# Kernel optimization log

Measured on AMD Instinct MI355X. Metric: run time of the kernel, lower is better.

Reference implementation:

```python
import jax, jax.numpy as jnp
import numpy as np

N_NODES = 4096   # nodes in propagation tree
WORDS = 64       # word indices per node (bag-of-words)
HID = 256        # hidden_dim
VOCAB = 50257    # word_dim
NCLASS = 4
N_LEAF = 2048


def setup_inputs() -> dict:
    key = jax.random.key(0)
    ks = jax.random.split(key, 16)
    s = jnp.float32(0.1)  # init_matrix scale
    tree = jax.random.randint(ks[0], (N_NODES, WORDS), 0, VOCAB, dtype=jnp.int32)
    # parent[i] < i so node_h[parent] is already computed (topological order)
    parent = jax.random.randint(ks[1], (N_NODES,), 0, N_NODES, dtype=jnp.int32)
    parent = jnp.minimum(parent, jnp.maximum(jnp.arange(N_NODES, dtype=jnp.int32) - 1, 0))
    edge = jnp.stack([parent, jnp.arange(N_NODES, dtype=jnp.int32)], axis=1)
    leaf_idxs = jax.random.randint(ks[2], (N_LEAF,), 0, N_NODES, dtype=jnp.int32)
    y = jax.random.uniform(ks[3], (NCLASS,), dtype=jnp.float32)
    E = jax.random.normal(ks[4], (HID, VOCAB), dtype=jnp.float32) * s
    W_z = jax.random.normal(ks[5], (HID, HID), dtype=jnp.float32) * s
    U_z = jax.random.normal(ks[6], (HID, HID), dtype=jnp.float32) * s
    W_r = jax.random.normal(ks[7], (HID, HID), dtype=jnp.float32) * s
    U_r = jax.random.normal(ks[8], (HID, HID), dtype=jnp.float32) * s
    W_h = jax.random.normal(ks[9], (HID, HID), dtype=jnp.float32) * s
    U_h = jax.random.normal(ks[10], (HID, HID), dtype=jnp.float32) * s
    W_out = jax.random.normal(ks[11], (NCLASS, HID), dtype=jnp.float32) * s
    b_z = jnp.zeros((HID,), jnp.float32)
    b_r = jnp.zeros((HID,), jnp.float32)
    b_h = jnp.zeros((HID,), jnp.float32)
    b_out = jnp.zeros((NCLASS,), jnp.float32)
    return dict(tree=tree, edge=edge, leaf_idxs=leaf_idxs, y=y, E=E,
                W_z=W_z, U_z=U_z, b_z=b_z, W_r=W_r, U_r=U_r, b_r=b_r,
                W_h=W_h, U_h=U_h, b_h=b_h, W_out=W_out, b_out=b_out)


def reference(tree, edge, leaf_idxs, y, E, W_z, U_z, b_z, W_r, U_r, b_r,
              W_h, U_h, b_h, W_out, b_out):
    n_nodes = tree.shape[0]
    # child_xe per node: sum of word embeddings -> [N, HID]
    X = jnp.take(E, tree, axis=1).sum(axis=-1).T
    # W.mul(x).sum(dim=1) == W @ x; precompute input-side matvecs for all nodes
    WzX = X @ W_z.T
    WrX = X @ W_r.T
    WhX = X @ W_h.T
    node_h0 = jnp.zeros((n_nodes, X.shape[1]), X.dtype).at[0].set(X[0])

    def step(node_h, inp):
        i, wzx, wrx, whx, p = inp
        ph = node_h[p]  # parent hidden state
        z = jax.nn.sigmoid(wzx + U_z @ ph + b_z)
        r = jax.nn.sigmoid(wrx + U_r @ ph + b_r)
        c = jnp.tanh(whx + U_h @ (ph * r) + b_h)
        h = z * ph + (1.0 - z) * c
        return node_h.at[i].set(h), None

    xs = (jnp.arange(1, n_nodes), WzX[1:], WrX[1:], WhX[1:], edge[1:, 0])
    node_h, _ = jax.lax.scan(step, node_h0, xs)
    final_state = node_h[leaf_idxs].max(axis=0)  # [HID]
    pred = jax.nn.softmax(W_out @ final_state + b_out)
    loss = jnp.sum((y - pred) ** 2)
    return pred, loss
```

## Files before the change

### kernel.cpp

```cpp
#include <hip/hip_runtime.h>
#include <math.h>

#define N_NODES 4096
#define WORDS   64
#define HID     256
#define VOCAB   50257
#define NCLASS  4
#define N_LEAF  2048
#define RNN_BLOCKS 256
#define POISON 0x7FFF7FFFu

typedef _Float16 half2_t __attribute__((ext_vector_type(2)));

__device__ __forceinline__ float dot2f(half2_t a, half2_t b, float c) {
#if __has_builtin(__builtin_amdgcn_fdot2)
  return __builtin_amdgcn_fdot2(a, b, c, false);
#else
  return c + (float)a.x * (float)b.x + (float)a.y * (float)b.y;
#endif
}

__device__ __forceinline__ half2_t f2h2(float f) {
  union { float f; half2_t h; } u; u.f = f; return u.h;
}

__device__ __forceinline__ float fast_rcp(float x) { return __builtin_amdgcn_rcpf(x); }
__device__ __forceinline__ float fast_sigmoid(float x) {
  return fast_rcp(1.f + __expf(-x));
}
__device__ __forceinline__ float fast_tanh(float x) {
  return 1.f - 2.f * fast_rcp(1.f + __expf(2.f * x));
}
__device__ __forceinline__ half2_t pkrtz(float a, float b) {
#if __has_builtin(__builtin_amdgcn_cvt_pkrtz)
  return __builtin_bit_cast(half2_t, __builtin_amdgcn_cvt_pkrtz(a, b));
#else
  half2_t v; v.x = (_Float16)a; v.y = (_Float16)b; return v;
#endif
}

__global__ void poison_hpk_kernel(unsigned* __restrict__ HpkU) {
  int i = blockIdx.x * blockDim.x + threadIdx.x;
  if (i < N_NODES * (HID / 2)) HpkU[i] = POISON;
}

__global__ void transpose_f16_kernel(const float* __restrict__ src, _Float16* __restrict__ dst,
                                     int R, int C) {
  __shared__ float tile[32][33];
  int c0 = blockIdx.x * 32, r0 = blockIdx.y * 32;
  int tx = threadIdx.x, ty = threadIdx.y;
#pragma unroll
  for (int j = 0; j < 32; j += 8) {
    int c = c0 + tx, r = r0 + ty + j;
    if (c < C) tile[ty + j][tx] = src[(size_t)r * C + c];
  }
  __syncthreads();
#pragma unroll
  for (int j = 0; j < 32; j += 8) {
    int c = c0 + ty + j, r = r0 + tx;
    if (c < C) dst[(size_t)c * R + r] = (_Float16)tile[tx][ty + j];
  }
}

__global__ void __launch_bounds__(256) pack_u_kernel(
    const float* __restrict__ Uz, const float* __restrict__ Ur, const float* __restrict__ Uh,
    half2_t* __restrict__ Upk) {
  __shared__ float tile[64][259];
  int m = blockIdx.x >> 2, g = blockIdx.x & 3;
  const float* U = m == 0 ? Uz : (m == 1 ? Ur : Uh);
  int t = threadIdx.x;
  for (int r = 0; r < 64; ++r) tile[r][t] = U[(size_t)(g * 64 + r) * 256 + t];
  __syncthreads();
#pragma unroll
  for (int it = 0; it < 32; ++it) {
    int e = it * 256 + t;
    int hl = e & 63, kj = e >> 6, s = kj >> 5, j = kj & 31;
    half2_t v;
    v.x = (_Float16)tile[hl][s * 64 + 2 * j];
    v.y = (_Float16)tile[hl][s * 64 + 2 * j + 1];
    Upk[(size_t)(m * 4 + s) * 8192 + j * 256 + (g * 64 + hl)] = v;
  }
}

__global__ void gather_x_kernel(const int* __restrict__ tree, const half2_t* __restrict__ ETh2,
                                float* __restrict__ X, float* __restrict__ H,
                                half2_t* __restrict__ Hpk) {
  int i = blockIdx.x;
  int t = threadIdx.x;
  __shared__ int vs[WORDS];
  if (t < WORDS) vs[t] = tree[i * WORDS + t];
  __syncthreads();
  float ax = 0.f, ay = 0.f;
#pragma unroll 8
  for (int w = 0; w < WORDS; ++w) {
    half2_t e = ETh2[(size_t)vs[w] * (HID / 2) + t];
    ax += (float)e.x;
    ay += (float)e.y;
  }
  float2 v2; v2.x = ax; v2.y = ay;
  ((float2*)(X + (size_t)i * HID))[t] = v2;
  if (i == 0) {
    ((float2*)H)[t] = v2;
    half2_t hv; hv.x = (_Float16)ax; hv.y = (_Float16)ay;
    Hpk[t] = hv;
  }
}

__global__ void __launch_bounds__(256) gemm3_kernel(
    const float* __restrict__ X,
    const float* __restrict__ W0, const float* __restrict__ W1, const float* __restrict__ W2,
    float* __restrict__ A0, float* __restrict__ A1, float* __restrict__ A2) {
  const float* W = blockIdx.z == 0 ? W0 : (blockIdx.z == 1 ? W1 : W2);
  float*       A = blockIdx.z == 0 ? A0 : (blockIdx.z == 1 ? A1 : A2);
  __shared__ float Xs[16][65];
  __shared__ float Ws[16][65];
  int tid = threadIdx.x;
  int m0 = blockIdx.x * 64, n0 = blockIdx.y * 64;
  int tm = (tid / 16) * 4, tn = (tid % 16) * 4;
  int lm = tid >> 2, lk = (tid & 3) * 4;
  float acc[4][4];
#pragma unroll
  for (int a = 0; a < 4; ++a)
#pragma unroll
    for (int b = 0; b < 4; ++b) acc[a][b] = 0.f;

  for (int k0 = 0; k0 < HID; k0 += 16) {
    float4 xv = *(const float4*)(X + (size_t)(m0 + lm) * HID + k0 + lk);
    Xs[lk + 0][lm] = xv.x; Xs[lk + 1][lm] = xv.y; Xs[lk + 2][lm] = xv.z; Xs[lk + 3][lm] = xv.w;
    float4 wv = *(const float4*)(W + (size_t)(n0 + lm) * HID + k0 + lk);
    Ws[lk + 0][lm] = wv.x; Ws[lk + 1][lm] = wv.y; Ws[lk + 2][lm] = wv.z; Ws[lk + 3][lm] = wv.w;
    __syncthreads();
#pragma unroll
    for (int k = 0; k < 16; ++k) {
      float xm[4], wn[4];
#pragma unroll
      for (int u = 0; u < 4; ++u) { xm[u] = Xs[k][tm + u]; wn[u] = Ws[k][tn + u]; }
#pragma unroll
      for (int a = 0; a < 4; ++a)
#pragma unroll
        for (int b = 0; b < 4; ++b) acc[a][b] = fmaf(xm[a], wn[b], acc[a][b]);
    }
    __syncthreads();
  }
#pragma unroll
  for (int a = 0; a < 4; ++a)
#pragma unroll
    for (int b = 0; b < 4; ++b)
      A[(size_t)(m0 + tm + a) * HID + n0 + tn + b] = acc[a][b];
}

__global__ void
__attribute__((amdgpu_flat_work_group_size(512, 512), amdgpu_waves_per_eu(2, 2)))
rnn_kernel(
    const float* __restrict__ Az, const float* __restrict__ Ar, const float* __restrict__ Ah,
    const half2_t* __restrict__ Upk,
    const float* __restrict__ bz, const float* __restrict__ br, const float* __restrict__ bh,
    const int* __restrict__ edge, float* __restrict__ H, unsigned* HpkU) {
  const int tid = threadIdx.x;
  const int h   = tid & (HID - 1);
  const int ks  = tid >> 8;
  __shared__ half2_t php[HID / 2];
  __shared__ half2_t rhp[HID / 2];
  __shared__ float   part[2 * HID];

  half2_t um[128];
  half2_t uhh[64];
  {
    const half2_t* mb = Upk + (size_t)(ks ? 4 : 0) * 8192 + h;
#pragma unroll
    for (int j = 0; j < 128; ++j)
      um[j] = mb[(j >> 5) * 8192 + (j & 31) * 256];
    const half2_t* hb = Upk + (size_t)(8 + 2 * ks) * 8192 + h;
#pragma unroll
    for (int j = 0; j < 64; ++j)
      uhh[j] = hb[(j >> 5) * 8192 + (j & 31) * 256];
  }
  const float b1  = ks ? br[h] : bz[h];
  const float bhv = ks ? 0.f : bh[h];

  const int istart = blockIdx.x == 0 ? RNN_BLOCKS : blockIdx.x;
  for (int i = istart; i < N_NODES; i += RNN_BLOCKS) {
    const int p = edge[2 * i];
    const float a1 = ks ? Ar[(size_t)i * HID + h] : Az[(size_t)i * HID + h];
    const float a2 = ks ? 0.f : Ah[(size_t)i * HID + h];

    if (tid < HID / 2) {
      unsigned v = __hip_atomic_load(&HpkU[(size_t)p * (HID / 2) + tid],
                                     __ATOMIC_RELAXED, __HIP_MEMORY_SCOPE_AGENT);
      long spin = 0;
      while (v == POISON) {
        if (++spin > (1L << 26)) break;
        v = __hip_atomic_load(&HpkU[(size_t)p * (HID / 2) + tid],
                              __ATOMIC_RELAXED, __HIP_MEMORY_SCOPE_AGENT);
      }
      php[tid] = __builtin_bit_cast(half2_t, v);
    }
    __syncthreads();

    half2_t ph2 = php[h >> 1];
    const float phv = (float)((h & 1) ? ph2.y : ph2.x);

    float ac0 = a1 + b1, ac1 = 0.f, ac2 = 0.f, ac3 = 0.f;
    {
      const float4* phq = (const float4*)php;
#pragma unroll
      for (int q = 0; q < 32; ++q) {
        float4 blk = phq[q];
        ac0 = dot2f(um[4 * q + 0], f2h2(blk.x), ac0);
        ac1 = dot2f(um[4 * q + 1], f2h2(blk.y), ac1);
        ac2 = dot2f(um[4 * q + 2], f2h2(blk.z), ac2);
        ac3 = dot2f(um[4 * q + 3], f2h2(blk.w), ac3);
      }
    }
    const float g = fast_sigmoid((ac0 + ac1) + (ac2 + ac3));
    if (ks) {
      float rh = g * phv;
      float nb = __shfl_xor(rh, 1, 64);
      if ((h & 1) == 0) rhp[h >> 1] = pkrtz(rh, nb);
    }
    __syncthreads();

    float c0 = 0.f, c1 = 0.f;
    {
      const float4* rq = (const float4*)(rhp + ks * 64);
#pragma unroll
      for (int q = 0; q < 16; ++q) {
        float4 blk = rq[q];
        c0 = dot2f(uhh[4 * q + 0], f2h2(blk.x), c0);
        c1 = dot2f(uhh[4 * q + 1], f2h2(blk.y), c1);
        c0 = dot2f(uhh[4 * q + 2], f2h2(blk.z), c0);
        c1 = dot2f(uhh[4 * q + 3], f2h2(blk.w), c1);
      }
    }
    part[ks * HID + h] = c0 + c1;
    __syncthreads();

    if (ks == 0) {
      float ca = a2 + bhv + part[h] + part[HID + h];
      float c  = fast_tanh(ca);
      float hn = fmaf(g, phv, (1.f - g) * c);
      float nb = __shfl_xor(hn, 1, 64);
      if ((h & 1) == 0) {
        __hip_atomic_store(&HpkU[(size_t)i * (HID / 2) + (h >> 1)],
                           __builtin_bit_cast(unsigned, pkrtz(hn, nb)),
                           __ATOMIC_RELAXED, __HIP_MEMORY_SCOPE_AGENT);
      }
      H[(size_t)i * HID + h] = hn;
    }
  }
}

__global__ void leafmax_kernel(const float* __restrict__ H, const int* __restrict__ leafs,
                               float* __restrict__ partial) {
  int b = blockIdx.x;
  int h = threadIdx.x;
  float m = -INFINITY;
#pragma unroll 4
  for (int j = 0; j < N_LEAF / 64; ++j) {
    int node = leafs[b * (N_LEAF / 64) + j];
    m = fmaxf(m, H[(size_t)node * HID + h]);
  }
  partial[b * HID + h] = m;
}

__global__ void final_kernel(const float* __restrict__ partial, const float* __restrict__ W_out,
                             const float* __restrict__ b_out, const float* __restrict__ y,
                             float* __restrict__ out) {
  int h = threadIdx.x;
  float m = -INFINITY;
#pragma unroll 8
  for (int b = 0; b < 64; ++b) m = fmaxf(m, partial[b * HID + h]);
  __shared__ float fs[HID];
  __shared__ float red[HID];
  __shared__ float logit[NCLASS];
  fs[h] = m;
  __syncthreads();
  for (int c = 0; c < NCLASS; ++c) {
    red[h] = W_out[c * HID + h] * fs[h];
    __syncthreads();
    for (int s = HID / 2; s > 0; s >>= 1) {
      if (h < s) red[h] += red[h + s];
      __syncthreads();
    }
    if (h == 0) logit[c] = red[0] + b_out[c];
    __syncthreads();
  }
  if (h == 0) {
    float mx = logit[0];
    for (int c = 1; c < NCLASS; ++c) mx = fmaxf(mx, logit[c]);
    float e[NCLASS], s = 0.f;
    for (int c = 0; c < NCLASS; ++c) { e[c] = expf(logit[c] - mx); s += e[c]; }
    float loss = 0.f;
    for (int c = 0; c < NCLASS; ++c) {
      float p = e[c] / s;
      out[c] = p;
      float d = y[c] - p;
      loss += d * d;
    }
    out[NCLASS] = loss;
  }
}

extern "C" void kernel_launch(void* const* d_in, const int* in_sizes, int n_in,
                              void* d_out, int out_size, void* d_ws, size_t ws_size,
                              hipStream_t stream) {
  const int*   tree = (const int*)d_in[0];
  const int*   edge = (const int*)d_in[1];
  const int*   leaf = (const int*)d_in[2];
  const float* y    = (const float*)d_in[3];
  const float* E    = (const float*)d_in[4];
  const float* Wz   = (const float*)d_in[5];
  const float* Uz   = (const float*)d_in[6];
  const float* bz   = (const float*)d_in[7];
  const float* Wr   = (const float*)d_in[8];
  const float* Ur   = (const float*)d_in[9];
  const float* br   = (const float*)d_in[10];
  const float* Wh   = (const float*)d_in[11];
  const float* Uh   = (const float*)d_in[12];
  const float* bh   = (const float*)d_in[13];
  const float* Wout = (const float*)d_in[14];
  const float* bout = (const float*)d_in[15];
  float* out = (float*)d_out;

  char* base = (char*)d_ws;
  size_t b = 0;
  _Float16* ETh = (_Float16*)(base + b); b += (size_t)VOCAB * HID * 2;
  b = (b + 255) & ~(size_t)255;
  half2_t* Upk = (half2_t*)(base + b); b += (size_t)3 * 4 * 8192 * 4;
  half2_t* Hpk = (half2_t*)(base + b); b += (size_t)N_NODES * (HID / 2) * 4;
  float* X   = (float*)(base + b); b += (size_t)N_NODES * HID * 4;
  float* Az  = (float*)(base + b); b += (size_t)N_NODES * HID * 4;
  float* Ar  = (float*)(base + b); b += (size_t)N_NODES * HID * 4;
  float* Ah  = (float*)(base + b); b += (size_t)N_NODES * HID * 4;
  float* H   = (float*)(base + b); b += (size_t)N_NODES * HID * 4;
  float* partial = (float*)(base + b); b += (size_t)64 * HID * 4;

  poison_hpk_kernel<<<(N_NODES * (HID / 2) + 255) / 256, 256, 0, stream>>>((unsigned*)Hpk);
  transpose_f16_kernel<<<dim3((VOCAB + 31) / 32, HID / 32), dim3(32, 8), 0, stream>>>(E, ETh, HID, VOCAB);
  pack_u_kernel<<<12, 256, 0, stream>>>(Uz, Ur, Uh, Upk);
  gather_x_kernel<<<N_NODES, 128, 0, stream>>>(tree, (const half2_t*)ETh, X, H, Hpk);
  gemm3_kernel<<<dim3(N_NODES / 64, HID / 64, 3), 256, 0, stream>>>(X, Wz, Wr, Wh, Az, Ar, Ah);
  rnn_kernel<<<RNN_BLOCKS, 512, 0, stream>>>(Az, Ar, Ah, Upk, bz, br, bh, edge, H, (unsigned*)Hpk);
  leafmax_kernel<<<64, HID, 0, stream>>>(H, leaf, partial);
  final_kernel<<<1, HID, 0, stream>>>(partial, Wout, bout, y, out);
}
```

Baseline: 538.4 us.

## Chain-follow consecutive child nodes in-block to bypass global spin handoff

After a block computes node j, it checks whether node j+1 has j as parent and has not yet been published. If so, it computes j+1 itself, reusing the just-computed hidden state from LDS instead of waiting for another block to poll it from global memory. Blocks also skip nodes that another block has already published. The intent is to shorten the sequential critical path on long parent chains by removing cross-block latency. The cost is extra atomic checks, redundant computation when two blocks race on the same node, and a sync hazard on the php rewrite.

```diff
diff --git a/kernel.cpp b/kernel.cpp
--- a/kernel.cpp
+++ b/kernel.cpp
@@ -162,6 +162,8 @@
   __shared__ half2_t php[HID / 2];
   __shared__ half2_t rhp[HID / 2];
   __shared__ float   part[2 * HID];
+  __shared__ int     sskip;
+  __shared__ int     sfol;
 
   half2_t um[128];
   half2_t uhh[64];
@@ -180,72 +182,100 @@
 
   const int istart = blockIdx.x == 0 ? RNN_BLOCKS : blockIdx.x;
   for (int i = istart; i < N_NODES; i += RNN_BLOCKS) {
-    const int p = edge[2 * i];
-    const float a1 = ks ? Ar[(size_t)i * HID + h] : Az[(size_t)i * HID + h];
-    const float a2 = ks ? 0.f : Ah[(size_t)i * HID + h];
-
-    if (tid < HID / 2) {
-      unsigned v = __hip_atomic_load(&HpkU[(size_t)p * (HID / 2) + tid],
-                                     __ATOMIC_RELAXED, __HIP_MEMORY_SCOPE_AGENT);
-      long spin = 0;
-      while (v == POISON) {
-        if (++spin > (1L << 26)) break;
-        v = __hip_atomic_load(&HpkU[(size_t)p * (HID / 2) + tid],
-                              __ATOMIC_RELAXED, __HIP_MEMORY_SCOPE_AGENT);
-      }
-      php[tid] = __builtin_bit_cast(half2_t, v);
-    }
-    __syncthreads();
-
-    half2_t ph2 = php[h >> 1];
-    const float phv = (float)((h & 1) ? ph2.y : ph2.x);
-
-    float ac0 = a1 + b1, ac1 = 0.f, ac2 = 0.f, ac3 = 0.f;
-    {
-      const float4* phq = (const float4*)php;
-#pragma unroll
-      for (int q = 0; q < 32; ++q) {
-        float4 blk = phq[q];
-        ac0 = dot2f(um[4 * q + 0], f2h2(blk.x), ac0);
-        ac1 = dot2f(um[4 * q + 1], f2h2(blk.y), ac1);
-        ac2 = dot2f(um[4 * q + 2], f2h2(blk.z), ac2);
-        ac3 = dot2f(um[4 * q + 3], f2h2(blk.w), ac3);
-      }
-    }
-    const float g = fast_sigmoid((ac0 + ac1) + (ac2 + ac3));
-    if (ks) {
-      float rh = g * phv;
-      float nb = __shfl_xor(rh, 1, 64);
-      if ((h & 1) == 0) rhp[h >> 1] = pkrtz(rh, nb);
-    }
-    __syncthreads();
-
-    float c0 = 0.f, c1 = 0.f;
-    {
-      const float4* rq = (const float4*)(rhp + ks * 64);
-#pragma unroll
-      for (int q = 0; q < 16; ++q) {
-        float4 blk = rq[q];
-        c0 = dot2f(uhh[4 * q + 0], f2h2(blk.x), c0);
-        c1 = dot2f(uhh[4 * q + 1], f2h2(blk.y), c1);
-        c0 = dot2f(uhh[4 * q + 2], f2h2(blk.z), c0);
-        c1 = dot2f(uhh[4 * q + 3], f2h2(blk.w), c1);
-      }
-    }
-    part[ks * HID + h] = c0 + c1;
-    __syncthreads();
-
-    if (ks == 0) {
-      float ca = a2 + bhv + part[h] + part[HID + h];
-      float c  = fast_tanh(ca);
-      float hn = fmaf(g, phv, (1.f - g) * c);
-      float nb = __shfl_xor(hn, 1, 64);
-      if ((h & 1) == 0) {
-        __hip_atomic_store(&HpkU[(size_t)i * (HID / 2) + (h >> 1)],
-                           __builtin_bit_cast(unsigned, pkrtz(hn, nb)),
-                           __ATOMIC_RELAXED, __HIP_MEMORY_SCOPE_AGENT);
-      }
-      H[(size_t)i * HID + h] = hn;
+    int j = i;
+    int p = edge[2 * j];
+    float a1 = ks ? Ar[(size_t)j * HID + h] : Az[(size_t)j * HID + h];
+    float a2 = ks ? 0.f : Ah[(size_t)j * HID + h];
+    bool useLds = false;
+
+    while (true) {
+      if (!useLds) {
+        if (tid == 0)
+          sskip = (__hip_atomic_load(&HpkU[(size_t)j * (HID / 2)],
+                                     __ATOMIC_RELAXED, __HIP_MEMORY_SCOPE_AGENT) != POISON);
+        if (tid < HID / 2) {
+          unsigned v = __hip_atomic_load(&HpkU[(size_t)p * (HID / 2) + tid],
+                                         __ATOMIC_RELAXED, __HIP_MEMORY_SCOPE_AGENT);
+          long spin = 0;
+          while (v == POISON) {
+            if (++spin > (1L << 26)) break;
+            v = __hip_atomic_load(&HpkU[(size_t)p * (HID / 2) + tid],
+                                  __ATOMIC_RELAXED, __HIP_MEMORY_SCOPE_AGENT);
+          }
+          php[tid] = __builtin_bit_cast(half2_t, v);
+        }
+      } else if (tid == 0) {
+        sskip = 0;
+      }
+      __syncthreads();
+      if (sskip) break;
+
+      const int jn = j + 1;
+      int pn = -1; unsigned pubw = 0u; float a1n = 0.f, a2n = 0.f;
+      if (jn < N_NODES) {
+        pn  = edge[2 * jn];
+        a1n = ks ? Ar[(size_t)jn * HID + h] : Az[(size_t)jn * HID + h];
+        a2n = ks ? 0.f : Ah[(size_t)jn * HID + h];
+        if (tid == 0)
+          pubw = __hip_atomic_load(&HpkU[(size_t)jn * (HID / 2)],
+                                   __ATOMIC_RELAXED, __HIP_MEMORY_SCOPE_AGENT);
+      }
+      if (tid == 0) sfol = (jn < N_NODES) && (pn == j) && (pubw == POISON);
+
+      half2_t ph2 = php[h >> 1];
+      const float phv = (float)((h & 1) ? ph2.y : ph2.x);
+
+      float ac0 = a1 + b1, ac1 = 0.f, ac2 = 0.f, ac3 = 0.f;
+      {
+        const float4* phq = (const float4*)php;
+#pragma unroll
+        for (int q = 0; q < 32; ++q) {
+          float4 blk = phq[q];
+          ac0 = dot2f(um[4 * q + 0], f2h2(blk.x), ac0);
+          ac1 = dot2f(um[4 * q + 1], f2h2(blk.y), ac1);
+          ac2 = dot2f(um[4 * q + 2], f2h2(blk.z), ac2);
+          ac3 = dot2f(um[4 * q + 3], f2h2(blk.w), ac3);
+        }
+      }
+      const float g = fast_sigmoid((ac0 + ac1) + (ac2 + ac3));
+      if (ks) {
+        float rh = g * phv;
+        float nb = __shfl_xor(rh, 1, 64);
+        if ((h & 1) == 0) rhp[h >> 1] = pkrtz(rh, nb);
+      }
+      __syncthreads();
+
+      float c0 = 0.f, c1 = 0.f;
+      {
+        const float4* rq = (const float4*)(rhp + ks * 64);
+#pragma unroll
+        for (int q = 0; q < 16; ++q) {
+          float4 blk = rq[q];
+          c0 = dot2f(uhh[4 * q + 0], f2h2(blk.x), c0);
+          c1 = dot2f(uhh[4 * q + 1], f2h2(blk.y), c1);
+          c0 = dot2f(uhh[4 * q + 2], f2h2(blk.z), c0);
+          c1 = dot2f(uhh[4 * q + 3], f2h2(blk.w), c1);
+        }
+      }
+      part[ks * HID + h] = c0 + c1;
+      __syncthreads();
+
+      const int fol = sfol;
+      if (ks == 0) {
+        float ca = a2 + bhv + part[h] + part[HID + h];
+        float c  = fast_tanh(ca);
+        float hn = fmaf(g, phv, (1.f - g) * c);
+        float nb = __shfl_xor(hn, 1, 64);
+        if ((h & 1) == 0) {
+          unsigned pk = __builtin_bit_cast(unsigned, pkrtz(hn, nb));
+          __hip_atomic_store(&HpkU[(size_t)j * (HID / 2) + (h >> 1)], pk,
+                             __ATOMIC_RELAXED, __HIP_MEMORY_SCOPE_AGENT);
+          if (fol) php[h >> 1] = __builtin_bit_cast(half2_t, pk);
+        }
+        H[(size_t)j * HID + h] = hn;
+      }
+      if (!fol) break;
+      j = jn; a1 = a1n; a2 = a2n; useLds = true;
     }
   }
 }
```

Measured after the change: 643.1 us. 1.19x slower.

## Repartition RNN gate work across half-blocks and prefetch next parent state

Applied to the files above, without the earlier changes.

The GRU step's matrix work is re-split between the two 256-thread halves. One half computes U_r and half of U_z, while the other computes the full U_h plus the other half of U_z. This removes the partial-sum reduction barrier, going from three syncthreads per step to two. The half that does not produce h now prefetches the next node's parent state, spinning on the poison flag, along with the next Ar, and the other half prefetches the next Az/Ah. This overlaps global latency with compute but risks load imbalance between the halves, and it lowers the spin timeout.

```diff
diff --git a/kernel.cpp b/kernel.cpp
--- a/kernel.cpp
+++ b/kernel.cpp
@@ -161,84 +161,106 @@
   const int ks  = tid >> 8;
   __shared__ half2_t php[HID / 2];
   __shared__ half2_t rhp[HID / 2];
-  __shared__ float   part[2 * HID];
-
-  half2_t um[128];
-  half2_t uhh[64];
+  __shared__ float   zh[HID];
+
+  half2_t big[128];
+  half2_t small[64];
   {
-    const half2_t* mb = Upk + (size_t)(ks ? 4 : 0) * 8192 + h;
+    const half2_t* mb = Upk + (size_t)(ks ? 4 : 8) * 8192 + h;
 #pragma unroll
     for (int j = 0; j < 128; ++j)
-      um[j] = mb[(j >> 5) * 8192 + (j & 31) * 256];
-    const half2_t* hb = Upk + (size_t)(8 + 2 * ks) * 8192 + h;
+      big[j] = mb[(j >> 5) * 8192 + (j & 31) * 256];
+    const half2_t* sb = Upk + (size_t)(ks ? 2 : 0) * 8192 + h;
 #pragma unroll
     for (int j = 0; j < 64; ++j)
-      uhh[j] = hb[(j >> 5) * 8192 + (j & 31) * 256];
-  }
-  const float b1  = ks ? br[h] : bz[h];
+      small[j] = sb[(j >> 5) * 8192 + (j & 31) * 256];
+  }
+  const float bzv = ks ? 0.f : bz[h];
   const float bhv = ks ? 0.f : bh[h];
-
-  const int istart = blockIdx.x == 0 ? RNN_BLOCKS : blockIdx.x;
-  for (int i = istart; i < N_NODES; i += RNN_BLOCKS) {
-    const int p = edge[2 * i];
-    const float a1 = ks ? Ar[(size_t)i * HID + h] : Az[(size_t)i * HID + h];
-    const float a2 = ks ? 0.f : Ah[(size_t)i * HID + h];
-
-    if (tid < HID / 2) {
-      unsigned v = __hip_atomic_load(&HpkU[(size_t)p * (HID / 2) + tid],
+  const float brv = ks ? br[h] : 0.f;
+
+  const int i0 = (blockIdx.x == 0) ? RNN_BLOCKS : blockIdx.x;
+  const int tl = tid - HID;
+
+  float az = 0.f, ah = 0.f, ar = 0.f;
+  if (!ks) {
+    az = Az[(size_t)i0 * HID + h];
+    ah = Ah[(size_t)i0 * HID + h];
+  } else {
+    ar = Ar[(size_t)i0 * HID + h];
+    const int p = edge[2 * i0];
+    if (tl < HID / 2) {
+      unsigned v = __hip_atomic_load(&HpkU[(size_t)p * (HID / 2) + tl],
                                      __ATOMIC_RELAXED, __HIP_MEMORY_SCOPE_AGENT);
       long spin = 0;
       while (v == POISON) {
-        if (++spin > (1L << 26)) break;
-        v = __hip_atomic_load(&HpkU[(size_t)p * (HID / 2) + tid],
+        if (++spin > (1L << 22)) break;
+        v = __hip_atomic_load(&HpkU[(size_t)p * (HID / 2) + tl],
                               __ATOMIC_RELAXED, __HIP_MEMORY_SCOPE_AGENT);
       }
-      php[tid] = __builtin_bit_cast(half2_t, v);
-    }
-    __syncthreads();
-
+      php[tl] = __builtin_bit_cast(half2_t, v);
+    }
+  }
+
+  for (int i = i0; i < N_NODES; i += RNN_BLOCKS) {
+    __syncthreads();
     half2_t ph2 = php[h >> 1];
     const float phv = (float)((h & 1) ? ph2.y : ph2.x);
-
-    float ac0 = a1 + b1, ac1 = 0.f, ac2 = 0.f, ac3 = 0.f;
-    {
-      const float4* phq = (const float4*)php;
+    const float4* phq = (const float4*)php;
+
+    float z0 = 0.f, z1 = 0.f, z2 = 0.f, z3 = 0.f;
+    float r0 = 0.f, r1 = 0.f, r2 = 0.f, r3 = 0.f;
+    if (ks) {
 #pragma unroll
       for (int q = 0; q < 32; ++q) {
         float4 blk = phq[q];
-        ac0 = dot2f(um[4 * q + 0], f2h2(blk.x), ac0);
-        ac1 = dot2f(um[4 * q + 1], f2h2(blk.y), ac1);
-        ac2 = dot2f(um[4 * q + 2], f2h2(blk.z), ac2);
-        ac3 = dot2f(um[4 * q + 3], f2h2(blk.w), ac3);
-      }
-    }
-    const float g = fast_sigmoid((ac0 + ac1) + (ac2 + ac3));
+        r0 = dot2f(big[4 * q + 0], f2h2(blk.x), r0);
+        r1 = dot2f(big[4 * q + 1], f2h2(blk.y), r1);
+        r2 = dot2f(big[4 * q + 2], f2h2(blk.z), r2);
+        r3 = dot2f(big[4 * q + 3], f2h2(blk.w), r3);
+      }
+    }
+    {
+      const int qo = ks ? 16 : 0;
+#pragma unroll
+      for (int q = 0; q < 16; ++q) {
+        float4 blk = phq[qo + q];
+        z0 = dot2f(small[4 * q + 0], f2h2(blk.x), z0);
+        z1 = dot2f(small[4 * q + 1], f2h2(blk.y), z1);
+        z2 = dot2f(small[4 * q + 2], f2h2(blk.z), z2);
+        z3 = dot2f(small[4 * q + 3], f2h2(blk.w), z3);
+      }
+    }
     if (ks) {
-      float rh = g * phv;
+      const float rg = fast_sigmoid(ar + brv + (r0 + r1) + (r2 + r3));
+      float rh = rg * phv;
       float nb = __shfl_xor(rh, 1, 64);
       if ((h & 1) == 0) rhp[h >> 1] = pkrtz(rh, nb);
-    }
-    __syncthreads();
-
-    float c0 = 0.f, c1 = 0.f;
-    {
-      const float4* rq = (const float4*)(rhp + ks * 64);
-#pragma unroll
-      for (int q = 0; q < 16; ++q) {
+      zh[h] = (z0 + z1) + (z2 + z3);
+    }
+    __syncthreads();
+
+    const int inext = i + RNN_BLOCKS;
+    if (!ks) {
+      const float zhi = zh[h];
+      float azn = 0.f, ahn = 0.f;
+      if (inext < N_NODES) {
+        azn = Az[(size_t)inext * HID + h];
+        ahn = Ah[(size_t)inext * HID + h];
+      }
+      const float4* rq = (const float4*)rhp;
+      float c0 = 0.f, c1 = 0.f, c2 = 0.f, c3 = 0.f;
+#pragma unroll
+      for (int q = 0; q < 32; ++q) {
         float4 blk = rq[q];
-        c0 = dot2f(uhh[4 * q + 0], f2h2(blk.x), c0);
-        c1 = dot2f(uhh[4 * q + 1], f2h2(blk.y), c1);
-        c0 = dot2f(uhh[4 * q + 2], f2h2(blk.z), c0);
-        c1 = dot2f(uhh[4 * q + 3], f2h2(blk.w), c1);
-      }
-    }
-    part[ks * HID + h] = c0 + c1;
-    __syncthreads();
-
-    if (ks == 0) {
-      float ca = a2 + bhv + part[h] + part[HID + h];
-      float c  = fast_tanh(ca);
-      float hn = fmaf(g, phv, (1.f - g) * c);
+        c0 = dot2f(big[4 * q + 0], f2h2(blk.x), c0);
+        c1 = dot2f(big[4 * q + 1], f2h2(blk.y), c1);
+        c2 = dot2f(big[4 * q + 2], f2h2(blk.z), c2);
+        c3 = dot2f(big[4 * q + 3], f2h2(blk.w), c3);
+      }
+      const float g  = fast_sigmoid(az + bzv + (z0 + z1) + (z2 + z3) + zhi);
+      const float c  = fast_tanh(ah + bhv + (c0 + c1) + (c2 + c3));
+      const float hn = fmaf(g, phv, (1.f - g) * c);
       float nb = __shfl_xor(hn, 1, 64);
       if ((h & 1) == 0) {
         __hip_atomic_store(&HpkU[(size_t)i * (HID / 2) + (h >> 1)],
@@ -246,6 +268,23 @@
                            __ATOMIC_RELAXED, __HIP_MEMORY_SCOPE_AGENT);
       }
       H[(size_t)i * HID + h] = hn;
+      az = azn; ah = ahn;
+    } else {
+      if (inext < N_NODES) {
+        ar = Ar[(size_t)inext * HID + h];
+        const int pn = edge[2 * inext];
+        if (tl < HID / 2) {
+          unsigned v = __hip_atomic_load(&HpkU[(size_t)pn * (HID / 2) + tl],
+                                         __ATOMIC_RELAXED, __HIP_MEMORY_SCOPE_AGENT);
+          long spin = 0;
+          while (v == POISON) {
+            if (++spin > (1L << 22)) break;
+            v = __hip_atomic_load(&HpkU[(size_t)pn * (HID / 2) + tl],
+                                  __ATOMIC_RELAXED, __HIP_MEMORY_SCOPE_AGENT);
+          }
+          php[tl] = __builtin_bit_cast(half2_t, v);
+        }
+      }
     }
   }
 }
```

Result: slower. 705.9 us (+31.1%).

## Fuse embedding gather with input-side W matvecs in one fp16 dot2 kernel

Applied to the files above, without the earlier changes.

Merges the bag-of-words gather and the three input-side W projections into one kernel. Each block handles four nodes, sums their embeddings into fp16 shared memory, then runs dot2 matvecs against packed fp16 W matrices that the pack kernel now also produces. This drops the fp32 X buffer round trip and one kernel launch. The cost is lower precision, since X and W are now fp16, and each block only reuses W across four nodes. It also lowers the spin-wait timeout in the RNN kernel.

```diff
diff --git a/kernel.cpp b/kernel.cpp
--- a/kernel.cpp
+++ b/kernel.cpp
@@ -64,10 +64,11 @@
 
 __global__ void __launch_bounds__(256) pack_u_kernel(
     const float* __restrict__ Uz, const float* __restrict__ Ur, const float* __restrict__ Uh,
+    const float* __restrict__ Wz, const float* __restrict__ Wr, const float* __restrict__ Wh,
     half2_t* __restrict__ Upk) {
   __shared__ float tile[64][259];
   int m = blockIdx.x >> 2, g = blockIdx.x & 3;
-  const float* U = m == 0 ? Uz : (m == 1 ? Ur : Uh);
+  const float* U = m == 0 ? Uz : (m == 1 ? Ur : (m == 2 ? Uh : (m == 3 ? Wz : (m == 4 ? Wr : Wh))));
   int t = threadIdx.x;
   for (int r = 0; r < 64; ++r) tile[r][t] = U[(size_t)(g * 64 + r) * 256 + t];
   __syncthreads();
@@ -82,71 +83,74 @@
   }
 }
 
-__global__ void gather_x_kernel(const int* __restrict__ tree, const half2_t* __restrict__ ETh2,
-                                float* __restrict__ X, float* __restrict__ H,
-                                half2_t* __restrict__ Hpk) {
-  int i = blockIdx.x;
-  int t = threadIdx.x;
-  __shared__ int vs[WORDS];
-  if (t < WORDS) vs[t] = tree[i * WORDS + t];
+__global__ void __launch_bounds__(256) gather_gemv_kernel(
+    const int* __restrict__ tree, const half2_t* __restrict__ ETh2,
+    const half2_t* __restrict__ Upk,
+    float* __restrict__ Az, float* __restrict__ Ar, float* __restrict__ Ah,
+    float* __restrict__ H, half2_t* __restrict__ Hpk) {
+  const int t  = threadIdx.x;
+  const int i0 = blockIdx.x * 4;
+  __shared__ int     vsf[4 * WORDS];
+  __shared__ float2  ps[256];
+  __shared__ half2_t Xh[4][HID / 2];
+
+  vsf[t] = tree[(size_t)i0 * WORDS + t];
   __syncthreads();
-  float ax = 0.f, ay = 0.f;
+
+  const int c    = t & 127;
+  const int half = t >> 7;
+#pragma unroll
+  for (int n = 0; n < 4; ++n) {
+    float ax = 0.f, ay = 0.f;
+    const int base = n * WORDS + half * 32;
 #pragma unroll 8
-  for (int w = 0; w < WORDS; ++w) {
-    half2_t e = ETh2[(size_t)vs[w] * (HID / 2) + t];
-    ax += (float)e.x;
-    ay += (float)e.y;
-  }
-  float2 v2; v2.x = ax; v2.y = ay;
-  ((float2*)(X + (size_t)i * HID))[t] = v2;
-  if (i == 0) {
-    ((float2*)H)[t] = v2;
-    half2_t hv; hv.x = (_Float16)ax; hv.y = (_Float16)ay;
-    Hpk[t] = hv;
-  }
-}
-
-__global__ void __launch_bounds__(256) gemm3_kernel(
-    const float* __restrict__ X,
-    const float* __restrict__ W0, const float* __restrict__ W1, const float* __restrict__ W2,
-    float* __restrict__ A0, float* __restrict__ A1, float* __restrict__ A2) {
-  const float* W = blockIdx.z == 0 ? W0 : (blockIdx.z == 1 ? W1 : W2);
-  float*       A = blockIdx.z == 0 ? A0 : (blockIdx.z == 1 ? A1 : A2);
-  __shared__ float Xs[16][65];
-  __shared__ float Ws[16][65];
-  int tid = threadIdx.x;
-  int m0 = blockIdx.x * 64, n0 = blockIdx.y * 64;
-  int tm = (tid / 16) * 4, tn = (tid % 16) * 4;
-  int lm = tid >> 2, lk = (tid & 3) * 4;
-  float acc[4][4];
-#pragma unroll
-  for (int a = 0; a < 4; ++a)
-#pragma unroll
-    for (int b = 0; b < 4; ++b) acc[a][b] = 0.f;
-
-  for (int k0 = 0; k0 < HID; k0 += 16) {
-    float4 xv = *(const float4*)(X + (size_t)(m0 + lm) * HID + k0 + lk);
-    Xs[lk + 0][lm] = xv.x; Xs[lk + 1][lm] = xv.y; Xs[lk + 2][lm] = xv.z; Xs[lk + 3][lm] = xv.w;
-    float4 wv = *(const float4*)(W + (size_t)(n0 + lm) * HID + k0 + lk);
-    Ws[lk + 0][lm] = wv.x; Ws[lk + 1][lm] = wv.y; Ws[lk + 2][lm] = wv.z; Ws[lk + 3][lm] = wv.w;
-    __syncthreads();
-#pragma unroll
-    for (int k = 0; k < 16; ++k) {
-      float xm[4], wn[4];
-#pragma unroll
-      for (int u = 0; u < 4; ++u) { xm[u] = Xs[k][tm + u]; wn[u] = Ws[k][tn + u]; }
-#pragma unroll
-      for (int a = 0; a < 4; ++a)
-#pragma unroll
-        for (int b = 0; b < 4; ++b) acc[a][b] = fmaf(xm[a], wn[b], acc[a][b]);
-    }
-    __syncthreads();
-  }
-#pragma unroll
-  for (int a = 0; a < 4; ++a)
-#pragma unroll
-    for (int b = 0; b < 4; ++b)
-      A[(size_t)(m0 + tm + a) * HID + n0 + tn + b] = acc[a][b];
+    for (int w = 0; w < 32; ++w) {
+      half2_t e = ETh2[(size_t)vsf[base + w] * (HID / 2) + c];
+      ax += (float)e.x;
+      ay += (float)e.y;
+    }
+    ps[t].x = ax; ps[t].y = ay;
+    __syncthreads();
+    if (t < 128) {
+      float xx = ps[t].x + ps[t + 128].x;
+      float yy = ps[t].y + ps[t + 128].y;
+      half2_t hv; hv.x = (_Float16)xx; hv.y = (_Float16)yy;
+      Xh[n][t] = hv;
+      if (i0 + n == 0) {
+        float2 v2; v2.x = xx; v2.y = yy;
+        ((float2*)H)[t] = v2;
+        Hpk[t] = hv;
+      }
+    }
+    __syncthreads();
+  }
+
+  float acc[3][4];
+#pragma unroll
+  for (int m = 0; m < 3; ++m)
+#pragma unroll
+    for (int n = 0; n < 4; ++n) acc[m][n] = 0.f;
+
+  const half2_t* wb = Upk + (size_t)12 * 8192 + t;
+#pragma unroll 8
+  for (int kp = 0; kp < 128; ++kp) {
+    half2_t w0 = wb[kp * 256];
+    half2_t w1 = wb[kp * 256 + 32768];
+    half2_t w2 = wb[kp * 256 + 65536];
+    half2_t x0 = Xh[0][kp], x1 = Xh[1][kp], x2 = Xh[2][kp], x3 = Xh[3][kp];
+    acc[0][0] = dot2f(w0, x0, acc[0][0]); acc[0][1] = dot2f(w0, x1, acc[0][1]);
+    acc[0][2] = dot2f(w0, x2, acc[0][2]); acc[0][3] = dot2f(w0, x3, acc[0][3]);
+    acc[1][0] = dot2f(w1, x0, acc[1][0]); acc[1][1] = dot2f(w1, x1, acc[1][1]);
+    acc[1][2] = dot2f(w1, x2, acc[1][2]); acc[1][3] = dot2f(w1, x3, acc[1][3]);
+    acc[2][0] = dot2f(w2, x0, acc[2][0]); acc[2][1] = dot2f(w2, x1, acc[2][1]);
+    acc[2][2] = dot2f(w2, x2, acc[2][2]); acc[2][3] = dot2f(w2, x3, acc[2][3]);
+  }
+#pragma unroll
+  for (int n = 0; n < 4; ++n) {
+    Az[(size_t)(i0 + n) * HID + t] = acc[0][n];
+    Ar[(size_t)(i0 + n) * HID + t] = acc[1][n];
+    Ah[(size_t)(i0 + n) * HID + t] = acc[2][n];
+  }
 }
 
 __global__ void
@@ -189,7 +193,7 @@
                                      __ATOMIC_RELAXED, __HIP_MEMORY_SCOPE_AGENT);
       long spin = 0;
       while (v == POISON) {
-        if (++spin > (1L << 26)) break;
+        if (++spin > (1L << 22)) break;
         v = __hip_atomic_load(&HpkU[(size_t)p * (HID / 2) + tid],
                               __ATOMIC_RELAXED, __HIP_MEMORY_SCOPE_AGENT);
       }
@@ -326,9 +330,8 @@
   size_t b = 0;
   _Float16* ETh = (_Float16*)(base + b); b += (size_t)VOCAB * HID * 2;
   b = (b + 255) & ~(size_t)255;
-  half2_t* Upk = (half2_t*)(base + b); b += (size_t)3 * 4 * 8192 * 4;
+  half2_t* Upk = (half2_t*)(base + b); b += (size_t)6 * 4 * 8192 * 4;
   half2_t* Hpk = (half2_t*)(base + b); b += (size_t)N_NODES * (HID / 2) * 4;
-  float* X   = (float*)(base + b); b += (size_t)N_NODES * HID * 4;
   float* Az  = (float*)(base + b); b += (size_t)N_NODES * HID * 4;
   float* Ar  = (float*)(base + b); b += (size_t)N_NODES * HID * 4;
   float* Ah  = (float*)(base + b); b += (size_t)N_NODES * HID * 4;
@@ -337,9 +340,9 @@
 
   poison_hpk_kernel<<<(N_NODES * (HID / 2) + 255) / 256, 256, 0, stream>>>((unsigned*)Hpk);
   transpose_f16_kernel<<<dim3((VOCAB + 31) / 32, HID / 32), dim3(32, 8), 0, stream>>>(E, ETh, HID, VOCAB);
-  pack_u_kernel<<<12, 256, 0, stream>>>(Uz, Ur, Uh, Upk);
-  gather_x_kernel<<<N_NODES, 128, 0, stream>>>(tree, (const half2_t*)ETh, X, H, Hpk);
-  gemm3_kernel<<<dim3(N_NODES / 64, HID / 64, 3), 256, 0, stream>>>(X, Wz, Wr, Wh, Az, Ar, Ah);
+  pack_u_kernel<<<24, 256, 0, stream>>>(Uz, Ur, Uh, Wz, Wr, Wh, Upk);
+  gather_gemv_kernel<<<N_NODES / 4, 256, 0, stream>>>(tree, (const half2_t*)ETh, Upk,
+                                                      Az, Ar, Ah, H, Hpk);
   rnn_kernel<<<RNN_BLOCKS, 512, 0, stream>>>(Az, Ar, Ah, Upk, bz, br, bh, edge, H, (unsigned*)Hpk);
   leafmax_kernel<<<64, HID, 0, stream>>>(H, leaf, partial);
   final_kernel<<<1, HID, 0, stream>>>(partial, Wout, bout, y, out);
```

Result: faster. 516.2 us (-4.1%).
